# Kernel tuning notes

Measured on AMD Instinct MI355X. Metric: run time of the kernel, lower is better.

## Reference

```python
import jax, jax.numpy as jnp
import numpy as np

N_NODES = 100000
N_EDGES = 1600000
D = 128  # conv_channels = [128, 128, 128] -> two GCNConv layers


def setup_inputs() -> dict:
    key = jax.random.key(0)
    ks = jax.random.split(key, 6)
    x = jax.random.normal(ks[0], (N_NODES, D), dtype=jnp.float32)
    edge_index = jax.random.randint(ks[1], (2, N_EDGES), 0, N_NODES, dtype=jnp.int32)
    s = 1.0 / np.sqrt(D)
    W1 = jax.random.uniform(ks[2], (D, D), jnp.float32, -s, s)
    b1 = jnp.zeros((D,), jnp.float32)
    W2 = jax.random.uniform(ks[3], (D, D), jnp.float32, -s, s)
    b2 = jnp.zeros((D,), jnp.float32)
    return {"x": x, "edge_index": edge_index, "W1": W1, "b1": b1, "W2": W2, "b2": b2}


def _gcn_layer(x, W, b, src, dst, norm, n_nodes):
    h = x @ W                       # [N, out]
    msg = h[src] * norm[:, None]    # gather + scale, [E', out]
    agg = jax.ops.segment_sum(msg, dst, num_segments=n_nodes)
    return agg + b


def reference(x, edge_index, W1, b1, W2, b2):
    n = x.shape[0]
    # add_self_loops: append (i, i) for every node
    loop = jnp.arange(n, dtype=edge_index.dtype)
    src = jnp.concatenate([edge_index[0], loop])
    dst = jnp.concatenate([edge_index[1], loop])
    # symmetric GCN normalization: deg over target nodes (unit edge weights)
    deg = jax.ops.segment_sum(jnp.ones_like(src, dtype=x.dtype), dst, num_segments=n)
    dis = jnp.where(deg > 0, jax.lax.rsqrt(deg), 0.0)
    norm = dis[src] * dis[dst]      # [E']

    h = _gcn_layer(x, W1, b1, src, dst, norm, n)
    h = jax.nn.elu(h)
    # dropout p=0.3 is identity in eval mode
    h = _gcn_layer(h, W2, b2, src, dst, norm, n)
    h = jax.nn.elu(h)
    return h
```

## Files before the change

### kernel.cpp

```cpp
#include <hip/hip_runtime.h>
#include <math.h>

#define NN 100000
#define NE 1600000
#define NT (NE + NN)
#define DD 128
#define NB 500
#define BR 200
#define BCAP 4096
#define NCH 2048
#define NBK 782
#define NBG 1563
#define PW 68
#define BMAGIC 21474837u

typedef unsigned int uint;
typedef unsigned short ushort;
typedef __attribute__((ext_vector_type(8))) short bf16x8;
typedef __attribute__((ext_vector_type(4))) float f32x4;

__device__ __forceinline__ uint bfr(float f){
  uint u = __float_as_uint(f);
  return (u + 0x7FFFu + ((u >> 16) & 1u)) >> 16;
}
__device__ __forceinline__ uint pk2(float a, float b){
  return (bfr(a) & 0xFFFFu) | (bfr(b) << 16);
}
__device__ __forceinline__ bf16x8 asbf(uint4 u){
  union { uint4 u; bf16x8 b; } c; c.u = u; return c.b;
}

__global__ __launch_bounds__(256) void k_init(const float* __restrict__ W1f, const float* __restrict__ W2f,
    uint* __restrict__ Wt1, uint* __restrict__ Wt2, int* __restrict__ gcnt){
  int t = threadIdx.x;
  if (blockIdx.x == 2){
    for (int i = t; i < 8000; i += 256) gcnt[i] = 0;
    return;
  }
  const float* W = blockIdx.x ? W2f : W1f;
  uint* Wt = blockIdx.x ? Wt2 : Wt1;
  int n = t >> 1, k0 = (t & 1) * 64;
  for (int kk = 0; kk < 64; kk += 2){
    float v0 = W[(size_t)(k0+kk  )*DD + n];
    float v1 = W[(size_t)(k0+kk+1)*DD + n];
    Wt[(size_t)n*64 + ((k0+kk)>>1)] = pk2(v0, v1);
  }
}


__global__ __launch_bounds__(256) void k_bucket(const int* __restrict__ ei,
    int* __restrict__ gcnt, uint* __restrict__ bedge){
  __shared__ uint   ent[NCH];
  __shared__ ushort bbs[NCH];
  __shared__ int    hist[NB];
  __shared__ int    fl[NB];
  __shared__ int    gb[NB];
  int t = threadIdx.x;
  int base = blockIdx.x * NCH;
  int nv = NE - base; if (nv > NCH) nv = NCH;
  for (int b = t; b < NB; b += 256){ hist[b] = 0; fl[b] = 0; }
  __syncthreads();
  for (int j = t; j < nv; j += 256){
    int i = base + j;
    uint s = (uint)ei[i];
    uint d = (uint)ei[NE + i];
    uint b = __umulhi(d, BMAGIC);
    uint dl = d - b*BR;
    ent[j] = s | (dl << 17);
    bbs[j] = (ushort)b;
    atomicAdd(&hist[b], 1);
  }
  __syncthreads();
  for (int b = t; b < NB; b += 256){
    int h = hist[b];
    gb[b] = h ? atomicAdd(&gcnt[b*16], h) : 0;
  }
  __syncthreads();
  for (int j = t; j < nv; j += 256){
    uint b = bbs[j];
    int q = atomicAdd(&fl[b], 1);
    bedge[(size_t)b*BCAP + gb[b] + q] = ent[j];
  }
}

__global__ __launch_bounds__(512) void k_bscan(const int* __restrict__ gcnt, int* __restrict__ bbase){
  __shared__ int s[512];
  int t = threadIdx.x;
  int v = (t < NB) ? (gcnt[t*16] + BR) : 0;
  s[t] = v;
  __syncthreads();
  for (int off = 1; off < 512; off <<= 1){
    int a = (t >= off) ? s[t-off] : 0;
    __syncthreads();
    s[t] += a;
    __syncthreads();
  }
  if (t < NB) bbase[t] = s[t] - v;
}

__global__ __launch_bounds__(256) void k_build(const int* __restrict__ gcnt,
    const int* __restrict__ bbase, const uint* __restrict__ bedge,
    float* __restrict__ dis, int* __restrict__ rowptr, uint* __restrict__ es){
  __shared__ uint eL[BCAP];
  __shared__ int  cl[BR];
  __shared__ int  fl[BR];
  __shared__ int  pf[256];
  int b = blockIdx.x, t = threadIdx.x;
  int base = bbase[b];
  if (t < BR){ cl[t] = 0; fl[t] = 0; }
  __syncthreads();
  int cnt = gcnt[b*16];
  for (int e = t; e < cnt; e += 256){
    uint u = bedge[(size_t)b*BCAP + e];
    eL[e] = u;
    atomicAdd(&cl[u >> 17], 1);
  }
  __syncthreads();
  int v = (t < BR) ? (cl[t] + 1) : 0;
  pf[t] = v;
  __syncthreads();
  for (int off = 1; off < 256; off <<= 1){
    int a = (t >= off) ? pf[t-off] : 0;
    __syncthreads();
    pf[t] += a;
    __syncthreads();
  }
  if (t < BR){
    int n  = b*BR + t;
    int p0 = base + pf[t] - v;
    rowptr[n] = p0;
    dis[n] = rsqrtf((float)(cl[t] + 1));
    es[p0 + cl[t]] = (uint)n;
  }
  if (b == NB-1 && t == 0) rowptr[NN] = NT;
  __syncthreads();
  for (int e = t; e < cnt; e += 256){
    uint u = eL[e];
    int  dloc = u >> 17;
    int  q  = atomicAdd(&fl[dloc], 1);
    int  p0 = base + pf[dloc] - (cl[dloc] + 1);
    es[p0 + q] = u & 0x1FFFFu;
  }
}

template<int IN_BF16>
__global__ __launch_bounds__(256, 3) void k_gemm(const void* __restrict__ Xv,
    const uint* __restrict__ Wt, const float* __restrict__ dis,
    uint* __restrict__ Y, int nrows){
  __shared__ uint Ws[128*PW];
  __shared__ uint Xs[64*PW];
  int t = threadIdx.x;
  int row0 = blockIdx.x * 64;

  #pragma unroll
  for (int it = 0; it < 8; ++it){
    int f = it*256 + t;
    uint4 v = ((const uint4*)Wt)[f];
    int row = f >> 4, c4 = f & 15;
    *(uint4*)&Ws[row*PW + c4*4] = v;
  }
  if (!IN_BF16){
    const float* X = (const float*)Xv;
    #pragma unroll
    for (int it = 0; it < 8; ++it){
      int f = it*256 + t;
      int row = f >> 5, c4 = f & 31;
      int gr = row0 + row;
      float4 v = (gr < nrows) ? ((const float4*)X)[(size_t)gr*32 + c4]
                              : make_float4(0.f,0.f,0.f,0.f);
      uint2 p; p.x = pk2(v.x, v.y); p.y = pk2(v.z, v.w);
      *(uint2*)&Xs[row*PW + c4*2] = p;
    }
  } else {
    const uint* X = (const uint*)Xv;
    #pragma unroll
    for (int it = 0; it < 4; ++it){
      int f = it*256 + t;
      int row = f >> 4, c4 = f & 15;
      int gr = row0 + row;
      uint4 v = (gr < nrows) ? ((const uint4*)X)[(size_t)gr*16 + c4]
                             : make_uint4(0,0,0,0);
      *(uint4*)&Xs[row*PW + c4*4] = v;
    }
  }
  __syncthreads();

  int wv = t >> 6, l = t & 63;
  int g = l >> 4, li = l & 15;
  int rb = wv*16 + li;
  int r  = row0 + rb;
  f32x4 acc[8];
  #pragma unroll
  for (int i = 0; i < 8; ++i) acc[i] = (f32x4){0.f,0.f,0.f,0.f};

  #pragma unroll
  for (int ks = 0; ks < 4; ++ks){
    int c = (ks*4 + g)*4;
    bf16x8 bfrag = asbf(*(const uint4*)&Xs[rb*PW + c]);
    #pragma unroll
    for (int nt = 0; nt < 8; ++nt){
      bf16x8 afrag = asbf(*(const uint4*)&Ws[(nt*16 + li)*PW + c]);
      acc[nt] = __builtin_amdgcn_mfma_f32_16x16x32_bf16(afrag, bfrag, acc[nt], 0, 0, 0);
    }
  }
  if (r < nrows){
    float dr = dis[r];
    #pragma unroll
    for (int nt = 0; nt < 8; ++nt){
      uint2 o;
      o.x = pk2(acc[nt][0]*dr, acc[nt][1]*dr);
      o.y = pk2(acc[nt][2]*dr, acc[nt][3]*dr);
      *(uint2*)&Y[(size_t)r*64 + nt*8 + g*2] = o;
    }
  }
}

template<int OUT_BF16>
__global__ __launch_bounds__(256) void k_agg(const uint* __restrict__ H,
    const int* __restrict__ rowptr, const float* __restrict__ dis,
    const uint* __restrict__ es, const float* __restrict__ bias,
    void* __restrict__ outv){
  int wid  = threadIdx.x >> 6;
  int lane = threadIdx.x & 63;
  int n = blockIdx.x*4 + wid;
  int e0 = rowptr[n];
  int e1 = rowptr[n+1];
  float a0 = 0.f, a1 = 0.f, a2 = 0.f, a3 = 0.f;
  int e = e0;

#define ASTEP(k,A,B) { uint s##k = es[e+k]; \
    uint h##k = H[(size_t)s##k*64 + lane]; \
    A += __uint_as_float(h##k << 16); \
    B += __uint_as_float(h##k & 0xFFFF0000u); }

  for (; e + 16 <= e1; e += 16){
    ASTEP( 0,a0,a1) ASTEP( 1,a2,a3) ASTEP( 2,a0,a1) ASTEP( 3,a2,a3)
    ASTEP( 4,a0,a1) ASTEP( 5,a2,a3) ASTEP( 6,a0,a1) ASTEP( 7,a2,a3)
    ASTEP( 8,a0,a1) ASTEP( 9,a2,a3) ASTEP(10,a0,a1) ASTEP(11,a2,a3)
    ASTEP(12,a0,a1) ASTEP(13,a2,a3) ASTEP(14,a0,a1) ASTEP(15,a2,a3)
  }
  for (; e + 4 <= e1; e += 4){
    ASTEP(0,a0,a1) ASTEP(1,a2,a3) ASTEP(2,a0,a1) ASTEP(3,a2,a3)
  }
  for (; e < e1; ++e){
    ASTEP(0,a0,a1)
  }
#undef ASTEP

  float dn = dis[n];
  float2 b = *(const float2*)&bias[lane*2];
  float v0 = fmaf(dn, a0 + a2, b.x);
  float v1 = fmaf(dn, a1 + a3, b.y);
  v0 = (v0 > 0.f) ? v0 : expm1f(v0);
  v1 = (v1 > 0.f) ? v1 : expm1f(v1);
  if (OUT_BF16){
    ((uint*)outv)[(size_t)n*64 + lane] = pk2(v0, v1);
  } else {
    float2 o; o.x = v0; o.y = v1;
    *(float2*)&((float*)outv)[(size_t)n*DD + lane*2] = o;
  }
}


extern "C" void kernel_launch(void* const* d_in, const int* in_sizes, int n_in,
                              void* d_out, int out_size, void* d_ws, size_t ws_size,
                              hipStream_t stream){
  const float* x  = (const float*)d_in[0];
  const int*   ei = (const int*)d_in[1];
  const float* W1 = (const float*)d_in[2];
  const float* b1 = (const float*)d_in[3];
  const float* W2 = (const float*)d_in[4];
  const float* b2 = (const float*)d_in[5];

  int*   ws_i   = (int*)d_ws;
  int*   gcnt   = ws_i + 0;
  int*   bbase  = ws_i + 8000;
  float* dis    = (float*)(ws_i + 8576);
  int*   rowptr = ws_i + 108608;
  uint*  Wt1    = (uint*)(ws_i + 208704);
  uint*  Wt2    = (uint*)(ws_i + 216896);
  uint*  es     = (uint*)(ws_i + 225088);
  uint*  bedge  = (uint*)(ws_i + 1925120);
  uint*  out1   = (uint*)(ws_i + 1925120);
  uint*  H      = (uint*)(ws_i + 8325120);
  uint*  H2     = H;

  k_init  <<<3,   256, 0, stream>>>(W1, W2, Wt1, Wt2, gcnt);
  k_bucket<<<NBK, 256, 0, stream>>>(ei, gcnt, bedge);
  k_bscan <<<1,   512, 0, stream>>>(gcnt, bbase);
  k_build <<<NB,  256, 0, stream>>>(gcnt, bbase, bedge, dis, rowptr, es);

  k_gemm<0><<<NBG, 256, 0, stream>>>(x, Wt1, dis, H, NN);
  k_agg<1> <<<25000, 256, 0, stream>>>(H, rowptr, dis, es, b1, out1);
  k_gemm<1><<<NBG, 256, 0, stream>>>(out1, Wt2, dis, H2, NN);
  k_agg<0> <<<25000, 256, 0, stream>>>(H2, rowptr, dis, es, b2, d_out);
}
```

Baseline: 243.3 us.

## Merge preprocessing kernels and overlap CSR build with first GEMM

Cuts the launch count by merging weight transpose with edge bucketing, and the bucket scan with per-node degree counting, into single kernels. It also runs the CSR scatter and the first-layer GEMM in one grid, using disjoint block ranges, so the two independent stages can overlap. The gcnt zeroing moves to hipMemsetAsync. The degree count is now a separate pass over bedge, which adds one extra read of the bucketed edges in exchange for fewer serialized launches.

```diff
diff --git a/kernel.cpp b/kernel.cpp
--- a/kernel.cpp
+++ b/kernel.cpp
@@ -30,33 +30,28 @@
   union { uint4 u; bf16x8 b; } c; c.u = u; return c.b;
 }
 
-__global__ __launch_bounds__(256) void k_init(const float* __restrict__ W1f, const float* __restrict__ W2f,
-    uint* __restrict__ Wt1, uint* __restrict__ Wt2, int* __restrict__ gcnt){
-  int t = threadIdx.x;
-  if (blockIdx.x == 2){
-    for (int i = t; i < 8000; i += 256) gcnt[i] = 0;
-    return;
-  }
-  const float* W = blockIdx.x ? W2f : W1f;
-  uint* Wt = blockIdx.x ? Wt2 : Wt1;
-  int n = t >> 1, k0 = (t & 1) * 64;
-  for (int kk = 0; kk < 64; kk += 2){
-    float v0 = W[(size_t)(k0+kk  )*DD + n];
-    float v1 = W[(size_t)(k0+kk+1)*DD + n];
-    Wt[(size_t)n*64 + ((k0+kk)>>1)] = pk2(v0, v1);
-  }
-}
-
-
-__global__ __launch_bounds__(256) void k_bucket(const int* __restrict__ ei,
-    int* __restrict__ gcnt, uint* __restrict__ bedge){
+__global__ __launch_bounds__(256) void k_pre1(const float* __restrict__ W1f, const float* __restrict__ W2f,
+    uint* __restrict__ Wt1, uint* __restrict__ Wt2,
+    const int* __restrict__ ei, int* __restrict__ gcnt, uint* __restrict__ bedge){
   __shared__ uint   ent[NCH];
   __shared__ ushort bbs[NCH];
   __shared__ int    hist[NB];
   __shared__ int    fl[NB];
   __shared__ int    gb[NB];
   int t = threadIdx.x;
-  int base = blockIdx.x * NCH;
+  if (blockIdx.x < 2){
+    const float* W = blockIdx.x ? W2f : W1f;
+    uint* Wt = blockIdx.x ? Wt2 : Wt1;
+    int n = t >> 1, k0 = (t & 1) * 64;
+    for (int kk = 0; kk < 64; kk += 2){
+      float v0 = W[(size_t)(k0+kk  )*DD + n];
+      float v1 = W[(size_t)(k0+kk+1)*DD + n];
+      Wt[(size_t)n*64 + ((k0+kk)>>1)] = pk2(v0, v1);
+    }
+    return;
+  }
+  int bid = blockIdx.x - 2;
+  int base = bid * NCH;
   int nv = NE - base; if (nv > NCH) nv = NCH;
   for (int b = t; b < NB; b += 256){ hist[b] = 0; fl[b] = 0; }
   __syncthreads();
@@ -83,75 +78,50 @@
   }
 }
 
-__global__ __launch_bounds__(512) void k_bscan(const int* __restrict__ gcnt, int* __restrict__ bbase){
-  __shared__ int s[512];
+__global__ __launch_bounds__(256) void k_pre2(const int* __restrict__ gcnt, int* __restrict__ bbase,
+    const uint* __restrict__ bedge, int* __restrict__ deg, float* __restrict__ dis){
+  __shared__ int sm[256];
   int t = threadIdx.x;
-  int v = (t < NB) ? (gcnt[t*16] + BR) : 0;
-  s[t] = v;
-  __syncthreads();
-  for (int off = 1; off < 512; off <<= 1){
-    int a = (t >= off) ? s[t-off] : 0;
+  if (blockIdx.x == 0){
+    int i0 = 2*t, i1 = 2*t + 1;
+    int v0 = (i0 < NB) ? (gcnt[i0*16] + BR) : 0;
+    int v1 = (i1 < NB) ? (gcnt[i1*16] + BR) : 0;
+    int p = v0 + v1;
+    sm[t] = p;
     __syncthreads();
-    s[t] += a;
-    __syncthreads();
-  }
-  if (t < NB) bbase[t] = s[t] - v;
-}
-
-__global__ __launch_bounds__(256) void k_build(const int* __restrict__ gcnt,
-    const int* __restrict__ bbase, const uint* __restrict__ bedge,
-    float* __restrict__ dis, int* __restrict__ rowptr, uint* __restrict__ es){
-  __shared__ uint eL[BCAP];
-  __shared__ int  cl[BR];
-  __shared__ int  fl[BR];
-  __shared__ int  pf[256];
-  int b = blockIdx.x, t = threadIdx.x;
-  int base = bbase[b];
-  if (t < BR){ cl[t] = 0; fl[t] = 0; }
+    for (int off = 1; off < 256; off <<= 1){
+      int a = (t >= off) ? sm[t-off] : 0;
+      __syncthreads();
+      sm[t] += a;
+      __syncthreads();
+    }
+    int excl = sm[t] - p;
+    if (i0 < NB) bbase[i0] = excl;
+    if (i1 < NB) bbase[i1] = excl + v0;
+    return;
+  }
+  int b = blockIdx.x - 1;
+  int* cl = sm;
+  if (t < BR) cl[t] = 0;
   __syncthreads();
   int cnt = gcnt[b*16];
   for (int e = t; e < cnt; e += 256){
-    uint u = bedge[(size_t)b*BCAP + e];
-    eL[e] = u;
-    atomicAdd(&cl[u >> 17], 1);
-  }
-  __syncthreads();
-  int v = (t < BR) ? (cl[t] + 1) : 0;
-  pf[t] = v;
-  __syncthreads();
-  for (int off = 1; off < 256; off <<= 1){
-    int a = (t >= off) ? pf[t-off] : 0;
-    __syncthreads();
-    pf[t] += a;
-    __syncthreads();
-  }
+    atomicAdd(&cl[bedge[(size_t)b*BCAP + e] >> 17], 1);
+  }
+  __syncthreads();
   if (t < BR){
-    int n  = b*BR + t;
-    int p0 = base + pf[t] - v;
-    rowptr[n] = p0;
-    dis[n] = rsqrtf((float)(cl[t] + 1));
-    es[p0 + cl[t]] = (uint)n;
-  }
-  if (b == NB-1 && t == 0) rowptr[NN] = NT;
-  __syncthreads();
-  for (int e = t; e < cnt; e += 256){
-    uint u = eL[e];
-    int  dloc = u >> 17;
-    int  q  = atomicAdd(&fl[dloc], 1);
-    int  p0 = base + pf[dloc] - (cl[dloc] + 1);
-    es[p0 + q] = u & 0x1FFFFu;
+    int n = b*BR + t;
+    int dg = cl[t];
+    deg[n] = dg;
+    dis[n] = rsqrtf((float)(dg + 1));
   }
 }
 
 template<int IN_BF16>
-__global__ __launch_bounds__(256, 3) void k_gemm(const void* __restrict__ Xv,
-    const uint* __restrict__ Wt, const float* __restrict__ dis,
-    uint* __restrict__ Y, int nrows){
-  __shared__ uint Ws[128*PW];
-  __shared__ uint Xs[64*PW];
+__device__ __forceinline__ void gemm_body(uint* __restrict__ Ws, uint* __restrict__ Xs,
+    const void* __restrict__ Xv, const uint* __restrict__ Wt,
+    const float* __restrict__ dis, uint* __restrict__ Y, int row0){
   int t = threadIdx.x;
-  int row0 = blockIdx.x * 64;
-
   #pragma unroll
   for (int it = 0; it < 8; ++it){
     int f = it*256 + t;
@@ -166,8 +136,8 @@
       int f = it*256 + t;
       int row = f >> 5, c4 = f & 31;
       int gr = row0 + row;
-      float4 v = (gr < nrows) ? ((const float4*)X)[(size_t)gr*32 + c4]
-                              : make_float4(0.f,0.f,0.f,0.f);
+      float4 v = (gr < NN) ? ((const float4*)X)[(size_t)gr*32 + c4]
+                           : make_float4(0.f,0.f,0.f,0.f);
       uint2 p; p.x = pk2(v.x, v.y); p.y = pk2(v.z, v.w);
       *(uint2*)&Xs[row*PW + c4*2] = p;
     }
@@ -178,8 +148,8 @@
       int f = it*256 + t;
       int row = f >> 4, c4 = f & 15;
       int gr = row0 + row;
-      uint4 v = (gr < nrows) ? ((const uint4*)X)[(size_t)gr*16 + c4]
-                             : make_uint4(0,0,0,0);
+      uint4 v = (gr < NN) ? ((const uint4*)X)[(size_t)gr*16 + c4]
+                          : make_uint4(0,0,0,0);
       *(uint4*)&Xs[row*PW + c4*4] = v;
     }
   }
@@ -203,7 +173,7 @@
       acc[nt] = __builtin_amdgcn_mfma_f32_16x16x32_bf16(afrag, bfrag, acc[nt], 0, 0, 0);
     }
   }
-  if (r < nrows){
+  if (r < NN){
     float dr = dis[r];
     #pragma unroll
     for (int nt = 0; nt < 8; ++nt){
@@ -213,6 +183,57 @@
       *(uint2*)&Y[(size_t)r*64 + nt*8 + g*2] = o;
     }
   }
+}
+
+__global__ __launch_bounds__(256, 3) void k_bg(const int* __restrict__ gcnt,
+    const int* __restrict__ bbase, const uint* __restrict__ bedge,
+    const int* __restrict__ deg, const float* __restrict__ dis,
+    int* __restrict__ rowptr, uint* __restrict__ es,
+    const float* __restrict__ X, const uint* __restrict__ Wt1, uint* __restrict__ H){
+  __shared__ uint smem[192*PW];
+  int t = threadIdx.x;
+  if (blockIdx.x >= NB){
+    gemm_body<0>(smem, smem + 128*PW, X, Wt1, dis, H, (blockIdx.x - NB)*64);
+    return;
+  }
+  int b = blockIdx.x;
+  int base = bbase[b];
+  int* cl = (int*)smem;
+  int* fl = cl + BR;
+  int* pf = cl + 2*BR;
+  if (t < BR){ cl[t] = deg[b*BR + t]; fl[t] = 0; }
+  __syncthreads();
+  int v = (t < BR) ? (cl[t] + 1) : 0;
+  pf[t] = v;
+  __syncthreads();
+  for (int off = 1; off < 256; off <<= 1){
+    int a = (t >= off) ? pf[t-off] : 0;
+    __syncthreads();
+    pf[t] += a;
+    __syncthreads();
+  }
+  if (t < BR){
+    int n  = b*BR + t;
+    int p0 = base + pf[t] - v;
+    rowptr[n] = p0;
+    es[p0 + cl[t]] = (uint)n;
+  }
+  if (b == NB-1 && t == 0) rowptr[NN] = NT;
+  __syncthreads();
+  int cnt = gcnt[b*16];
+  for (int e = t; e < cnt; e += 256){
+    uint u = bedge[(size_t)b*BCAP + e];
+    int  dloc = u >> 17;
+    int  q  = atomicAdd(&fl[dloc], 1);
+    int  p0 = base + pf[dloc] - (cl[dloc] + 1);
+    es[p0 + q] = u & 0x1FFFFu;
+  }
+}
+
+__global__ __launch_bounds__(256, 3) void k_gemm2(const uint* __restrict__ X,
+    const uint* __restrict__ Wt, const float* __restrict__ dis, uint* __restrict__ Y){
+  __shared__ uint smem[192*PW];
+  gemm_body<1>(smem, smem + 128*PW, X, Wt, dis, Y, blockIdx.x*64);
 }
 
 template<int OUT_BF16>
@@ -277,21 +298,21 @@
   int*   bbase  = ws_i + 8000;
   float* dis    = (float*)(ws_i + 8576);
   int*   rowptr = ws_i + 108608;
-  uint*  Wt1    = (uint*)(ws_i + 208704);
-  uint*  Wt2    = (uint*)(ws_i + 216896);
-  uint*  es     = (uint*)(ws_i + 225088);
-  uint*  bedge  = (uint*)(ws_i + 1925120);
-  uint*  out1   = (uint*)(ws_i + 1925120);
-  uint*  H      = (uint*)(ws_i + 8325120);
+  int*   deg    = ws_i + 208704;
+  uint*  Wt1    = (uint*)(ws_i + 308736);
+  uint*  Wt2    = (uint*)(ws_i + 316928);
+  uint*  es     = (uint*)(ws_i + 325120);
+  uint*  bedge  = (uint*)(ws_i + 2025152);
+  uint*  out1   = (uint*)(ws_i + 2025152);
+  uint*  H      = (uint*)(ws_i + 8425152);
   uint*  H2     = H;
 
-  k_init  <<<3,   256, 0, stream>>>(W1, W2, Wt1, Wt2, gcnt);
-  k_bucket<<<NBK, 256, 0, stream>>>(ei, gcnt, bedge);
-  k_bscan <<<1,   512, 0, stream>>>(gcnt, bbase);
-  k_build <<<NB,  256, 0, stream>>>(gcnt, bbase, bedge, dis, rowptr, es);
-
-  k_gemm<0><<<NBG, 256, 0, stream>>>(x, Wt1, dis, H, NN);
-  k_agg<1> <<<25000, 256, 0, stream>>>(H, rowptr, dis, es, b1, out1);
-  k_gemm<1><<<NBG, 256, 0, stream>>>(out1, Wt2, dis, H2, NN);
-  k_agg<0> <<<25000, 256, 0, stream>>>(H2, rowptr, dis, es, b2, d_out);
-}
+  hipMemsetAsync(gcnt, 0, 8000*sizeof(int), stream);
+
+  k_pre1<<<NBK + 2, 256, 0, stream>>>(W1, W2, Wt1, Wt2, ei, gcnt, bedge);
+  k_pre2<<<NB + 1,  256, 0, stream>>>(gcnt, bbase, bedge, deg, dis);
+  k_bg  <<<NB + NBG,256, 0, stream>>>(gcnt, bbase, bedge, deg, dis, rowptr, es, x, Wt1, H);
+  k_agg<1><<<25000, 256, 0, stream>>>(H, rowptr, dis, es, b1, out1);
+  k_gemm2 <<<NBG,   256, 0, stream>>>(out1, Wt2, dis, H2);
+  k_agg<0><<<25000, 256, 0, stream>>>(H2, rowptr, dis, es, b2, d_out);
+}
```

Result: faster. 233.7 us, median of 2 (-3.9%).
